# Kernel tuning notes

Hardware: AMD Instinct MI355X
Metric: run time of the kernel (lower is better)

## Reference

```python
import jax, jax.numpy as jnp
import numpy as np

B, L, D, H = 2, 2048, 1024, 16
HD = D // H


def _xavier(key, out_f, in_f):
    std = (2.0 / (in_f + out_f)) ** 0.5
    return jax.random.normal(key, (out_f, in_f), dtype=jnp.float32) * std


def setup_inputs() -> dict:
    key = jax.random.key(0)
    k = jax.random.split(key, 8)
    Q = jax.random.normal(k[0], (B, L, D), dtype=jnp.float32)
    K = jax.random.normal(k[1], (B, L, D), dtype=jnp.float32)
    V = jax.random.normal(k[2], (B, L, D), dtype=jnp.float32)
    mask = jnp.tril(jnp.ones((L, L), dtype=jnp.int32))[None, None]  # causal [1,1,L,L]
    wq = _xavier(k[3], D, D)
    wk = _xavier(k[4], D, D)
    wv = _xavier(k[5], D, D)
    wo = _xavier(k[6], D, D)
    bo = jnp.zeros((D,), dtype=jnp.float32)
    return {"Q": Q, "K": K, "V": V, "mask": mask,
            "wq": wq, "wk": wk, "wv": wv, "wo": wo, "bo": bo}


def reference(Q, K, V, mask, wq, wk, wv, wo, bo):
    N, Lq, Dm = Q.shape
    # projections: X @ W^T (Linear stores [out, in])
    q = (Q @ wq.T).reshape(N, Lq, H, HD).transpose(0, 2, 1, 3)  # [N,H,L,hd]
    kk = (K @ wk.T).reshape(N, Lq, H, HD).transpose(0, 2, 1, 3)
    v = (V @ wv.T).reshape(N, Lq, H, HD).transpose(0, 2, 1, 3)
    score = jnp.einsum('bhqd,bhkd->bhqk', q, kk) / jnp.sqrt(jnp.float32(HD))
    score = jnp.where(mask == 0, -jnp.inf, score)
    weights = jax.nn.softmax(score, axis=-1)
    attn = jnp.einsum('bhqk,bhkd->bhqd', weights, v)
    out = attn.transpose(0, 2, 1, 3).reshape(N, Lq, Dm)
    return out @ wo.T + bo
```

## Files before the change

### kernel.cpp

```cpp
#include <hip/hip_runtime.h>
#include <hip/hip_bf16.h>


#define B_ 2
#define L_ 2048
#define D_ 1024
#define H_ 16
#define HD_ 64
#define NA_ ((size_t)B_ * L_ * D_)
#define NW_ ((size_t)D_ * D_)

typedef __attribute__((ext_vector_type(8))) short bf16x8;
typedef __attribute__((ext_vector_type(4))) float f32x4;
typedef __hip_bfloat16 bf16;

__device__ __forceinline__ void async_load16(const void* g, void* l) {
  __builtin_amdgcn_global_load_lds((const __attribute__((address_space(1))) void*)g,
                                   (__attribute__((address_space(3))) void*)l,
                                   16, 0, 0);
}

__global__ __launch_bounds__(256) void xcvt_kernel(const float* __restrict__ q,
                                                   const float* __restrict__ k,
                                                   const float* __restrict__ v,
                                                   const float* __restrict__ w0,
                                                   const float* __restrict__ w1,
                                                   const float* __restrict__ w2,
                                                   const float* __restrict__ w3,
                                                   bf16* __restrict__ dst) {
  const int y = blockIdx.y;
  size_t i = ((size_t)blockIdx.x * 256 + threadIdx.x) * 4;
  const float* src;
  size_t soff = i;
  if (y < 3) {
    src = (y == 0) ? q : (y == 1) ? k : v;
  } else {
    int w = (int)(i >> 20);
    src = (w == 0) ? w0 : (w == 1) ? w1 : (w == 2) ? w2 : w3;
    soff = i & (NW_ - 1);
  }
  float4 vv = *(const float4*)(src + soff);
  union { bf16 h[4]; uint2 u; } pk;
  pk.h[0] = __float2bfloat16(vv.x);
  pk.h[1] = __float2bfloat16(vv.y);
  pk.h[2] = __float2bfloat16(vv.z);
  pk.h[3] = __float2bfloat16(vv.w);
  *(uint2*)(dst + (size_t)y * NA_ + i) = pk.u;
}

#define TS_ 136
__global__ __launch_bounds__(256) void gemm_qkv(const bf16* __restrict__ Qb,
                                                const bf16* __restrict__ Kb,
                                                const bf16* __restrict__ Vb,
                                                const bf16* __restrict__ Wb,
                                                bf16* __restrict__ qp,
                                                bf16* __restrict__ kp,
                                                bf16* __restrict__ vtp) {
  __shared__ __align__(16) bf16 smem[128 * TS_];
  bf16* As = smem;
  bf16* Bs = smem + 128 * 32;
  const int tid = threadIdx.x;
  const int wv = tid >> 6, lane = tid & 63;
  const int quad = lane >> 4, l16 = lane & 15;
  const int wm = wv & 1, wn = wv >> 1;
  const int m0 = blockIdx.x * 128, n0 = blockIdx.y * 128;
  const int z = blockIdx.z;
  const bf16* X = (z == 0) ? Qb : (z == 1) ? Kb : Vb;
  const bf16* W = Wb + (size_t)z * NW_;

  f32x4 acc[4][4];
#pragma unroll
  for (int i = 0; i < 4; i++)
#pragma unroll
    for (int j = 0; j < 4; j++) acc[i][j] = (f32x4){0.f, 0.f, 0.f, 0.f};

  for (int k0 = 0; k0 < D_; k0 += 32) {
#pragma unroll
    for (int it = 0; it < 2; it++) {
      int c = (wv * 2 + it) * 64 + lane;
      int row = c >> 2, cc = c & 3;
      async_load16(X + (size_t)(m0 + row) * D_ + k0 + cc * 8, (char*)As + c * 16);
      async_load16(W + (size_t)(n0 + row) * D_ + k0 + cc * 8, (char*)Bs + c * 16);
    }
    __syncthreads();
    bf16x8 af[4], bfr[4];
#pragma unroll
    for (int mi = 0; mi < 4; mi++)
      af[mi] = *(const bf16x8*)&As[(wm * 64 + mi * 16 + l16) * 32 + quad * 8];
#pragma unroll
    for (int ni = 0; ni < 4; ni++)
      bfr[ni] = *(const bf16x8*)&Bs[(wn * 64 + ni * 16 + l16) * 32 + quad * 8];
#pragma unroll
    for (int mi = 0; mi < 4; mi++)
#pragma unroll
      for (int ni = 0; ni < 4; ni++)
        acc[mi][ni] = __builtin_amdgcn_mfma_f32_16x16x32_bf16(af[mi], bfr[ni],
                                                              acc[mi][ni], 0, 0, 0);
    __syncthreads();
  }

  if (z == 2) {
    bf16* T = smem;
#pragma unroll
    for (int mi = 0; mi < 4; mi++) {
#pragma unroll
      for (int ni = 0; ni < 4; ni++) {
        int n_loc = wn * 64 + ni * 16 + l16;
        int m_loc = wm * 64 + mi * 16 + quad * 4;
        union { bf16 hx[4]; uint2 d; } pk;
#pragma unroll
        for (int r = 0; r < 4; r++) pk.hx[r] = __float2bfloat16(acc[mi][ni][r]);
        *(uint2*)&T[n_loc * TS_ + m_loc] = pk.d;
      }
    }
    __syncthreads();
#pragma unroll
    for (int p = 0; p < 8; p++) {
      int n_loc = p * 16 + (tid >> 4);
      int m_loc = (tid & 15) * 8;
      bf16x8 vv = *(const bf16x8*)&T[n_loc * TS_ + m_loc];
      int n = n0 + n_loc;
      int m = m0 + m_loc;
      int bb = m >> 11, l = m & (L_ - 1);
      int hh = n >> 6, hd = n & 63;
      *(bf16x8*)&vtp[((size_t)((bb * H_ + hh) * HD_ + hd)) * L_ + l] = vv;
    }
  } else {
    const float sc = (z == 0) ? 0.125f : 1.0f;
    bf16* dst = (z == 0) ? qp : kp;
#pragma unroll
    for (int mi = 0; mi < 4; mi++) {
#pragma unroll
      for (int ni = 0; ni < 4; ni++) {
        int n = n0 + wn * 64 + ni * 16 + l16;
#pragma unroll
        for (int r = 0; r < 4; r++) {
          int m = m0 + wm * 64 + mi * 16 + quad * 4 + r;
          dst[(size_t)m * D_ + n] = __float2bfloat16(acc[mi][ni][r] * sc);
        }
      }
    }
  }
}

__global__ __launch_bounds__(256) void attn_kernel(const bf16* __restrict__ qp,
                                                   const bf16* __restrict__ kp,
                                                   const bf16* __restrict__ vt,
                                                   bf16* __restrict__ attn) {
  __shared__ __align__(16) bf16 Kt[2][64 * 64];
  __shared__ __align__(16) bf16 Vt[2][64 * 64];
  __shared__ __align__(16) bf16 Pl[4][16 * 72];
  __shared__ __align__(16) bf16 Ph[4][16 * 72];
  const int tid = threadIdx.x;
  const int wv = tid >> 6, lane = tid & 63;
  const int quad = lane >> 4, l16 = lane & 15;
  const int pair = blockIdx.x, h = blockIdx.y, b = blockIdx.z;
  const int qlo = pair, qhi = (L_ / 64 - 1) - pair;

  const int rL = qlo * 64 + wv * 16 + l16;
  const int rH = qhi * 64 + wv * 16 + l16;
  bf16x8 qaL[2], qaH[2];
#pragma unroll
  for (int kk = 0; kk < 2; kk++) {
    qaL[kk] = *(const bf16x8*)&qp[((size_t)(b * L_ + rL)) * D_ + h * HD_ +
                                  kk * 32 + quad * 8];
    qaH[kk] = *(const bf16x8*)&qp[((size_t)(b * L_ + rH)) * D_ + h * HD_ +
                                  kk * 32 + quad * 8];
  }

  f32x4 OL[4], OH[4];
#pragma unroll
  for (int t = 0; t < 4; t++) {
    OL[t] = (f32x4){0.f, 0.f, 0.f, 0.f};
    OH[t] = (f32x4){0.f, 0.f, 0.f, 0.f};
  }
  float lL[4] = {0.f, 0.f, 0.f, 0.f}, lH[4] = {0.f, 0.f, 0.f, 0.f};

  const int csw = quad ^ (l16 & 7);

  auto stage = [&](int j, int buf) {
    const int j0 = j * 64;
#pragma unroll
    for (int it = 0; it < 2; it++) {
      int slot = (wv * 2 + it) * 64 + lane;
      int row = slot >> 3, c = (slot & 7) ^ (row & 7);
      async_load16(kp + ((size_t)(b * L_ + j0 + row)) * D_ + h * HD_ + c * 8,
                   (char*)Kt[buf] + slot * 16);
      async_load16(vt + ((size_t)((b * H_ + h) * HD_ + row)) * L_ + j0 + c * 8,
                   (char*)Vt[buf] + slot * 16);
    }
  };

  stage(0, 0);
  for (int j = 0; j <= qhi; j++) {
    const int buf = j & 1;
    const int j0 = j * 64;
    const bool doLo = (j <= qlo);
    __syncthreads();
    if (j < qhi) stage(j + 1, buf ^ 1);

    f32x4 sL[4], sH[4];
#pragma unroll
    for (int ss = 0; ss < 4; ss++) {
      int krow = ss * 16 + l16;
      bf16x8 kb0 = *(const bf16x8*)&Kt[buf][krow * 64 + csw * 8];
      bf16x8 kb1 = *(const bf16x8*)&Kt[buf][krow * 64 + (csw ^ 4) * 8];
      f32x4 s = (f32x4){0.f, 0.f, 0.f, 0.f};
      s = __builtin_amdgcn_mfma_f32_16x16x32_bf16(qaH[0], kb0, s, 0, 0, 0);
      s = __builtin_amdgcn_mfma_f32_16x16x32_bf16(qaH[1], kb1, s, 0, 0, 0);
      sH[ss] = s;
      if (doLo) {
        f32x4 t = (f32x4){0.f, 0.f, 0.f, 0.f};
        t = __builtin_amdgcn_mfma_f32_16x16x32_bf16(qaL[0], kb0, t, 0, 0, 0);
        t = __builtin_amdgcn_mfma_f32_16x16x32_bf16(qaL[1], kb1, t, 0, 0, 0);
        sL[ss] = t;
      }
    }

    if (j == qhi) {
#pragma unroll
      for (int ss = 0; ss < 4; ss++) {
        int key = j0 + ss * 16 + l16;
#pragma unroll
        for (int r = 0; r < 4; r++) {
          int rq = qhi * 64 + wv * 16 + quad * 4 + r;
          if (key > rq) sH[ss][r] = -1e30f;
        }
      }
    }
    if (doLo && j == qlo) {
#pragma unroll
      for (int ss = 0; ss < 4; ss++) {
        int key = j0 + ss * 16 + l16;
#pragma unroll
        for (int r = 0; r < 4; r++) {
          int rq = qlo * 64 + wv * 16 + quad * 4 + r;
          if (key > rq) sL[ss][r] = -1e30f;
        }
      }
    }
#pragma unroll
    for (int ss = 0; ss < 4; ss++) {
#pragma unroll
      for (int r = 0; r < 4; r++) {
        float p = __expf(sH[ss][r]);
        lH[r] += p;
        Ph[wv][(quad * 4 + r) * 72 + ss * 16 + l16] = __float2bfloat16(p);
      }
    }
    if (doLo) {
#pragma unroll
      for (int ss = 0; ss < 4; ss++) {
#pragma unroll
        for (int r = 0; r < 4; r++) {
          float p = __expf(sL[ss][r]);
          lL[r] += p;
          Pl[wv][(quad * 4 + r) * 72 + ss * 16 + l16] = __float2bfloat16(p);
        }
      }
    }

    asm volatile("s_waitcnt lgkmcnt(0)" ::: "memory");

#pragma unroll
    for (int kk = 0; kk < 2; kk++) {
      bf16x8 pah = *(const bf16x8*)&Ph[wv][l16 * 72 + kk * 32 + quad * 8];
      bf16x8 pal;
      if (doLo) pal = *(const bf16x8*)&Pl[wv][l16 * 72 + kk * 32 + quad * 8];
#pragma unroll
      for (int t = 0; t < 4; t++) {
        bf16x8 vb = *(const bf16x8*)&Vt[buf][(t * 16 + l16) * 64 + (csw ^ (kk * 4)) * 8];
        OH[t] = __builtin_amdgcn_mfma_f32_16x16x32_bf16(pah, vb, OH[t], 0, 0, 0);
        if (doLo) OL[t] = __builtin_amdgcn_mfma_f32_16x16x32_bf16(pal, vb, OL[t], 0, 0, 0);
      }
    }
  }

#pragma unroll
  for (int r = 0; r < 4; r++) {
#pragma unroll
    for (int off = 1; off < 16; off <<= 1) {
      lL[r] += __shfl_xor(lL[r], off, 64);
      lH[r] += __shfl_xor(lH[r], off, 64);
    }
  }
#pragma unroll
  for (int t = 0; t < 4; t++) {
#pragma unroll
    for (int r = 0; r < 4; r++) {
      int rowL = qlo * 64 + wv * 16 + quad * 4 + r;
      int rowH = qhi * 64 + wv * 16 + quad * 4 + r;
      attn[((size_t)(b * L_ + rowL)) * D_ + h * HD_ + t * 16 + l16] =
          __float2bfloat16(OL[t][r] / lL[r]);
      attn[((size_t)(b * L_ + rowH)) * D_ + h * HD_ + t * 16 + l16] =
          __float2bfloat16(OH[t][r] / lH[r]);
    }
  }
}

__global__ __launch_bounds__(256) void gemm_out(const bf16* __restrict__ X,
                                                const bf16* __restrict__ W,
                                                const float* __restrict__ bias,
                                                float* __restrict__ out) {
  __shared__ __align__(16) bf16 As[64 * 32];
  __shared__ __align__(16) bf16 Bs[128 * 32];
  const int tid = threadIdx.x;
  const int wv = tid >> 6, lane = tid & 63;
  const int quad = lane >> 4, l16 = lane & 15;
  const int wm = wv & 1, wn = wv >> 1;
  const int m0 = blockIdx.x * 64, n0 = blockIdx.y * 128;

  f32x4 acc[2][4];
#pragma unroll
  for (int i = 0; i < 2; i++)
#pragma unroll
    for (int j = 0; j < 4; j++) acc[i][j] = (f32x4){0.f, 0.f, 0.f, 0.f};

  for (int k0 = 0; k0 < D_; k0 += 32) {
    {
      int c = tid;
      int row = c >> 2, cc = c & 3;
      async_load16(X + (size_t)(m0 + row) * D_ + k0 + cc * 8, (char*)As + c * 16);
    }
#pragma unroll
    for (int it = 0; it < 2; it++) {
      int c = (wv * 2 + it) * 64 + lane;
      int row = c >> 2, cc = c & 3;
      async_load16(W + (size_t)(n0 + row) * D_ + k0 + cc * 8, (char*)Bs + c * 16);
    }
    __syncthreads();
    bf16x8 af[2], bfr[4];
#pragma unroll
    for (int mi = 0; mi < 2; mi++)
      af[mi] = *(const bf16x8*)&As[(wm * 32 + mi * 16 + l16) * 32 + quad * 8];
#pragma unroll
    for (int ni = 0; ni < 4; ni++)
      bfr[ni] = *(const bf16x8*)&Bs[(wn * 64 + ni * 16 + l16) * 32 + quad * 8];
#pragma unroll
    for (int mi = 0; mi < 2; mi++)
#pragma unroll
      for (int ni = 0; ni < 4; ni++)
        acc[mi][ni] = __builtin_amdgcn_mfma_f32_16x16x32_bf16(af[mi], bfr[ni],
                                                              acc[mi][ni], 0, 0, 0);
    __syncthreads();
  }

#pragma unroll
  for (int mi = 0; mi < 2; mi++) {
#pragma unroll
    for (int ni = 0; ni < 4; ni++) {
      int n = n0 + wn * 64 + ni * 16 + l16;
      float bval = bias[n];
#pragma unroll
      for (int r = 0; r < 4; r++) {
        int m = m0 + wm * 32 + mi * 16 + quad * 4 + r;
        out[(size_t)m * D_ + n] = acc[mi][ni][r] + bval;
      }
    }
  }
}

extern "C" void kernel_launch(void* const* d_in, const int* in_sizes, int n_in,
                              void* d_out, int out_size, void* d_ws, size_t ws_size,
                              hipStream_t stream) {
  const float* Q  = (const float*)d_in[0];
  const float* K  = (const float*)d_in[1];
  const float* V  = (const float*)d_in[2];
  const float* wq = (const float*)d_in[4];
  const float* wk = (const float*)d_in[5];
  const float* wvp = (const float*)d_in[6];
  const float* wo = (const float*)d_in[7];
  const float* bo = (const float*)d_in[8];
  float* out = (float*)d_out;

  bf16* base = (bf16*)d_ws;
  bf16* Qb = base;
  bf16* Kb = Qb + NA_;
  bf16* Vb = Kb + NA_;
  bf16* Wb = Vb + NA_;
  bf16* qp = Wb + 4 * NW_;
  bf16* kp = qp + NA_;
  bf16* vt = kp + NA_;
  bf16* at = vt + NA_;

  xcvt_kernel<<<dim3(NA_ / 1024, 4), 256, 0, stream>>>(Q, K, V, wq, wk, wvp, wo, base);
  gemm_qkv<<<dim3(32, 8, 3), 256, 0, stream>>>(Qb, Kb, Vb, Wb, qp, kp, vt);
  attn_kernel<<<dim3(L_ / 128, H_, B_), 256, 0, stream>>>(qp, kp, vt, at);
  gemm_out<<<dim3(64, 8), 256, 0, stream>>>(at, Wb + 3 * NW_, bo, out);
}
```

Before: 232.1 us.

## Split paired causal attention blocks into one query band per block, heaviest first

Replaces the lo/hi paired query-tile scheme with one 64-row query band per block, launched in reverse band order so the longest causal bands are scheduled first. The QK^T MFMA operands are swapped so each lane holds a query column, which lets it pack four probabilities into one 8-byte LDS store and keep a single scalar row-sum reduced by two shuffles. This doubles the block count and drops the doLo branches and the second P buffer, aiming for better occupancy and load balance. In exchange, each K/V tile is loaded once per band rather than shared by two query tiles, so global/LDS traffic for K/V rises.

```diff
diff --git a/kernel.cpp b/kernel.cpp
--- a/kernel.cpp
+++ b/kernel.cpp
@@ -149,32 +149,23 @@
                                                    bf16* __restrict__ attn) {
   __shared__ __align__(16) bf16 Kt[2][64 * 64];
   __shared__ __align__(16) bf16 Vt[2][64 * 64];
-  __shared__ __align__(16) bf16 Pl[4][16 * 72];
-  __shared__ __align__(16) bf16 Ph[4][16 * 72];
+  __shared__ __align__(16) bf16 P[4][16 * 72];
   const int tid = threadIdx.x;
   const int wv = tid >> 6, lane = tid & 63;
   const int quad = lane >> 4, l16 = lane & 15;
-  const int pair = blockIdx.x, h = blockIdx.y, b = blockIdx.z;
-  const int qlo = pair, qhi = (L_ / 64 - 1) - pair;
-
-  const int rL = qlo * 64 + wv * 16 + l16;
-  const int rH = qhi * 64 + wv * 16 + l16;
-  bf16x8 qaL[2], qaH[2];
-#pragma unroll
-  for (int kk = 0; kk < 2; kk++) {
-    qaL[kk] = *(const bf16x8*)&qp[((size_t)(b * L_ + rL)) * D_ + h * HD_ +
-                                  kk * 32 + quad * 8];
-    qaH[kk] = *(const bf16x8*)&qp[((size_t)(b * L_ + rH)) * D_ + h * HD_ +
-                                  kk * 32 + quad * 8];
-  }
-
-  f32x4 OL[4], OH[4];
-#pragma unroll
-  for (int t = 0; t < 4; t++) {
-    OL[t] = (f32x4){0.f, 0.f, 0.f, 0.f};
-    OH[t] = (f32x4){0.f, 0.f, 0.f, 0.f};
-  }
-  float lL[4] = {0.f, 0.f, 0.f, 0.f}, lH[4] = {0.f, 0.f, 0.f, 0.f};
+  const int h = blockIdx.x, band = 31 - (int)blockIdx.y, b = blockIdx.z;
+
+  const int rq = band * 64 + wv * 16 + l16;
+  bf16x8 qa[2];
+#pragma unroll
+  for (int kk = 0; kk < 2; kk++)
+    qa[kk] = *(const bf16x8*)&qp[((size_t)(b * L_ + rq)) * D_ + h * HD_ +
+                                 kk * 32 + quad * 8];
+
+  f32x4 O[4];
+#pragma unroll
+  for (int t = 0; t < 4; t++) O[t] = (f32x4){0.f, 0.f, 0.f, 0.f};
+  float l = 0.f;
 
   const int csw = quad ^ (l16 & 7);
 
@@ -192,108 +183,73 @@
   };
 
   stage(0, 0);
-  for (int j = 0; j <= qhi; j++) {
+  for (int j = 0; j <= band; j++) {
     const int buf = j & 1;
     const int j0 = j * 64;
-    const bool doLo = (j <= qlo);
-    __syncthreads();
-    if (j < qhi) stage(j + 1, buf ^ 1);
-
-    f32x4 sL[4], sH[4];
+    __syncthreads();
+    if (j < band) stage(j + 1, buf ^ 1);
+
+    f32x4 s[4];
 #pragma unroll
     for (int ss = 0; ss < 4; ss++) {
       int krow = ss * 16 + l16;
       bf16x8 kb0 = *(const bf16x8*)&Kt[buf][krow * 64 + csw * 8];
       bf16x8 kb1 = *(const bf16x8*)&Kt[buf][krow * 64 + (csw ^ 4) * 8];
-      f32x4 s = (f32x4){0.f, 0.f, 0.f, 0.f};
-      s = __builtin_amdgcn_mfma_f32_16x16x32_bf16(qaH[0], kb0, s, 0, 0, 0);
-      s = __builtin_amdgcn_mfma_f32_16x16x32_bf16(qaH[1], kb1, s, 0, 0, 0);
-      sH[ss] = s;
-      if (doLo) {
-        f32x4 t = (f32x4){0.f, 0.f, 0.f, 0.f};
-        t = __builtin_amdgcn_mfma_f32_16x16x32_bf16(qaL[0], kb0, t, 0, 0, 0);
-        t = __builtin_amdgcn_mfma_f32_16x16x32_bf16(qaL[1], kb1, t, 0, 0, 0);
-        sL[ss] = t;
-      }
-    }
-
-    if (j == qhi) {
-#pragma unroll
-      for (int ss = 0; ss < 4; ss++) {
-        int key = j0 + ss * 16 + l16;
+      f32x4 t = (f32x4){0.f, 0.f, 0.f, 0.f};
+      t = __builtin_amdgcn_mfma_f32_16x16x32_bf16(kb0, qa[0], t, 0, 0, 0);
+      t = __builtin_amdgcn_mfma_f32_16x16x32_bf16(kb1, qa[1], t, 0, 0, 0);
+      s[ss] = t;
+    }
+
+    if (j == band) {
+#pragma unroll
+      for (int ss = 0; ss < 4; ss++)
 #pragma unroll
         for (int r = 0; r < 4; r++) {
-          int rq = qhi * 64 + wv * 16 + quad * 4 + r;
-          if (key > rq) sH[ss][r] = -1e30f;
+          int key = j0 + ss * 16 + quad * 4 + r;
+          if (key > rq) s[ss][r] = -1e30f;
         }
-      }
-    }
-    if (doLo && j == qlo) {
-#pragma unroll
-      for (int ss = 0; ss < 4; ss++) {
-        int key = j0 + ss * 16 + l16;
-#pragma unroll
-        for (int r = 0; r < 4; r++) {
-          int rq = qlo * 64 + wv * 16 + quad * 4 + r;
-          if (key > rq) sL[ss][r] = -1e30f;
-        }
-      }
-    }
+    }
+
 #pragma unroll
     for (int ss = 0; ss < 4; ss++) {
-#pragma unroll
-      for (int r = 0; r < 4; r++) {
-        float p = __expf(sH[ss][r]);
-        lH[r] += p;
-        Ph[wv][(quad * 4 + r) * 72 + ss * 16 + l16] = __float2bfloat16(p);
-      }
-    }
-    if (doLo) {
-#pragma unroll
-      for (int ss = 0; ss < 4; ss++) {
-#pragma unroll
-        for (int r = 0; r < 4; r++) {
-          float p = __expf(sL[ss][r]);
-          lL[r] += p;
-          Pl[wv][(quad * 4 + r) * 72 + ss * 16 + l16] = __float2bfloat16(p);
-        }
-      }
+      float p0 = __expf(s[ss][0]), p1 = __expf(s[ss][1]);
+      float p2 = __expf(s[ss][2]), p3 = __expf(s[ss][3]);
+      l += (p0 + p1) + (p2 + p3);
+      union { bf16 hx[4]; uint2 d; } pk;
+      pk.hx[0] = __float2bfloat16(p0);
+      pk.hx[1] = __float2bfloat16(p1);
+      pk.hx[2] = __float2bfloat16(p2);
+      pk.hx[3] = __float2bfloat16(p3);
+      *(uint2*)&P[wv][l16 * 72 + ss * 16 + quad * 4] = pk.d;
     }
 
     asm volatile("s_waitcnt lgkmcnt(0)" ::: "memory");
 
 #pragma unroll
     for (int kk = 0; kk < 2; kk++) {
-      bf16x8 pah = *(const bf16x8*)&Ph[wv][l16 * 72 + kk * 32 + quad * 8];
-      bf16x8 pal;
-      if (doLo) pal = *(const bf16x8*)&Pl[wv][l16 * 72 + kk * 32 + quad * 8];
+      bf16x8 pa = *(const bf16x8*)&P[wv][l16 * 72 + kk * 32 + quad * 8];
 #pragma unroll
       for (int t = 0; t < 4; t++) {
         bf16x8 vb = *(const bf16x8*)&Vt[buf][(t * 16 + l16) * 64 + (csw ^ (kk * 4)) * 8];
-        OH[t] = __builtin_amdgcn_mfma_f32_16x16x32_bf16(pah, vb, OH[t], 0, 0, 0);
-        if (doLo) OL[t] = __builtin_amdgcn_mfma_f32_16x16x32_bf16(pal, vb, OL[t], 0, 0, 0);
+        O[t] = __builtin_amdgcn_mfma_f32_16x16x32_bf16(pa, vb, O[t], 0, 0, 0);
       }
     }
   }
 
-#pragma unroll
-  for (int r = 0; r < 4; r++) {
-#pragma unroll
-    for (int off = 1; off < 16; off <<= 1) {
-      lL[r] += __shfl_xor(lL[r], off, 64);
-      lH[r] += __shfl_xor(lH[r], off, 64);
-    }
-  }
+  l += __shfl_xor(l, 16, 64);
+  l += __shfl_xor(l, 32, 64);
+  float lq[4];
+#pragma unroll
+  for (int r = 0; r < 4; r++) lq[r] = __shfl(l, quad * 4 + r, 64);
+
 #pragma unroll
   for (int t = 0; t < 4; t++) {
 #pragma unroll
     for (int r = 0; r < 4; r++) {
-      int rowL = qlo * 64 + wv * 16 + quad * 4 + r;
-      int rowH = qhi * 64 + wv * 16 + quad * 4 + r;
-      attn[((size_t)(b * L_ + rowL)) * D_ + h * HD_ + t * 16 + l16] =
-          __float2bfloat16(OL[t][r] / lL[r]);
-      attn[((size_t)(b * L_ + rowH)) * D_ + h * HD_ + t * 16 + l16] =
-          __float2bfloat16(OH[t][r] / lH[r]);
+      int row = band * 64 + wv * 16 + quad * 4 + r;
+      attn[((size_t)(b * L_ + row)) * D_ + h * HD_ + t * 16 + l16] =
+          __float2bfloat16(O[t][r] / lq[r]);
     }
   }
 }
@@ -385,6 +341,6 @@
 
   xcvt_kernel<<<dim3(NA_ / 1024, 4), 256, 0, stream>>>(Q, K, V, wq, wk, wvp, wo, base);
   gemm_qkv<<<dim3(32, 8, 3), 256, 0, stream>>>(Qb, Kb, Vb, Wb, qp, kp, vt);
-  attn_kernel<<<dim3(L_ / 128, H_, B_), 256, 0, stream>>>(qp, kp, vt, at);
+  attn_kernel<<<dim3(H_, L_ / 64, B_), 256, 0, stream>>>(qp, kp, vt, at);
   gemm_out<<<dim3(64, 8), 256, 0, stream>>>(at, Wb + 3 * NW_, bo, out);
 }
```

Result: faster. 218.7 us (-5.8%).
